# Kernel optimization log

Hardware: AMD Instinct MI355X
Metric: run time of the kernel (lower is better)

## Reference

```python
import jax, jax.numpy as jnp
import numpy as np

N_QUBITS = 12
DIM = 2 ** N_QUBITS  # 4096

_H = (jnp.array([[1.0, 1.0], [1.0, -1.0]]) / np.sqrt(2.0)).astype(jnp.complex64)
_X = jnp.array([[0.0, 1.0], [1.0, 0.0]], dtype=jnp.complex64)


def setup_inputs() -> dict:
    key = jax.random.key(0)
    k1, k2 = jax.random.split(key)
    state = jax.random.normal(k1, (8, 512, DIM), dtype=jnp.float32)
    params = jax.random.normal(k2, (N_QUBITS,), dtype=jnp.float32)
    return {"state": state, "params": params}


def _to_quantum(x):
    # faithful to _classical_to_quantum_inspired: normalize, phase = acos(|v|), sign * exp(i*phase)
    norms = jnp.linalg.norm(x, axis=-1, keepdims=True)
    v = x / (norms + 1e-8)
    mag = jnp.minimum(jnp.abs(v), 1.0)
    q = (jnp.sign(v) * jnp.exp(1j * jnp.arccos(mag))).astype(jnp.complex64)
    nrm = jnp.sqrt(jnp.sum(q.real ** 2 + q.imag ** 2, axis=-1, keepdims=True))
    return q / nrm.astype(jnp.complex64)


def _axis(q):
    # qubit q = bit q (LSB); tensor axes ordered MSB-first after batch axis 0
    return 1 + (N_QUBITS - 1 - q)


def _apply_1q(full, q, U):
    ax = _axis(q)
    moved = jnp.moveaxis(full, ax, -1)
    out = jnp.einsum('...b,ab->...a', moved, U)
    return jnp.moveaxis(out, -1, ax)


def _apply_ctrl(full, c, t, U):
    # apply U on target qubit t where control qubit c == 1
    axc = _axis(c)
    b0 = jnp.take(full, 0, axis=axc)
    b1 = jnp.take(full, 1, axis=axc)
    axt = _axis(t)
    axt_sub = axt - 1 if axt > axc else axt
    moved = jnp.moveaxis(b1, axt_sub, -1)
    b1n = jnp.moveaxis(jnp.einsum('...b,ab->...a', moved, U), -1, axt_sub)
    return jnp.stack([b0, b1n], axis=axc)


def _rx(theta):
    c = jnp.cos(theta / 2).astype(jnp.complex64)
    s = (-1j * jnp.sin(theta / 2)).astype(jnp.complex64)
    return jnp.stack([jnp.stack([c, s]), jnp.stack([s, c])])


def reference(state, params):
    B, T, D = state.shape
    psi = _to_quantum(state.reshape(B * T, D))  # (N, 2**n) complex64
    full = psi.reshape((B * T,) + (2,) * N_QUBITS)
    for q in range(N_QUBITS):
        full = _apply_1q(full, q, _H)                                  # Hadamard
        full = _apply_ctrl(full, q, (q + 1) % N_QUBITS, _rx(params[q]))  # controlled-RX
        if q < N_QUBITS - 1:
            full = _apply_ctrl(full, q, q + 1, _X)                     # CNOT
    amp = full.reshape(B * T, D)
    probs = amp.real ** 2 + amp.imag ** 2  # measurement probabilities
    return probs.reshape(B, T, D).astype(jnp.float32)
```

## Files before the change

kernel.cpp:

```cpp
#include <hip/hip_runtime.h>

#define NQ  12
#define DIM 4096
#define TPB 256

typedef float v2f __attribute__((ext_vector_type(2)));
typedef float v4f __attribute__((ext_vector_type(4)));


__device__ __forceinline__ float wave_reduce(float v) {
#pragma unroll
    for (int m = 32; m >= 1; m >>= 1) v += __shfl_xor(v, m, 64);
    return v;
}

#define BCAST(v, q) __uint_as_float(__builtin_amdgcn_readlane(__float_as_uint(v), (q)))

template <int MC, int MT, bool XGATE>
__device__ __forceinline__ void apply_layer(v2f* a, v2f ctv, v2f snv) {
#pragma unroll
    for (int i = 0; i < 16; ++i) {
        if (i & MC) continue;
        const int j = i | MC;
        const v2f t0 = a[i], t1 = a[j];
        a[i] = t0 + t1;
        a[j] = t0 - t1;
    }
#pragma unroll
    for (int i = 0; i < 16; ++i) {
        if (!(i & MC) || (i & MT)) continue;
        const int j = i | MT;
        const v2f b0 = a[i], b1 = a[j];
        const v2f s0 = snv * b0.yx;
        const v2f s1 = snv * b1.yx;
        if (XGATE) {
            a[i] = ctv * b1 + s0;
            a[j] = ctv * b0 + s1;
        } else {
            a[i] = ctv * b0 + s1;
            a[j] = ctv * b1 + s0;
        }
    }
}

__global__ __launch_bounds__(TPB, 4) void qlayer_kernel(
        const float* __restrict__ state, const float* __restrict__ params,
        float* __restrict__ out) {
    __shared__ __align__(16) v2f amp[DIM + 256];
    __shared__ float red[4];

    const int t = threadIdx.x;
    const int lane = t & 63;
    const long long sbase = (long long)blockIdx.x * DIM;

    const float th = params[lane < NQ ? lane : 0] * 0.5f;
    const float cl = cosf(th);
    const float sl = sinf(th);

    float x[16];
    const float4* gp = (const float4*)(state + sbase + t * 16);
    float ss = 0.f;
#pragma unroll
    for (int j = 0; j < 4; ++j) {
        const float4 v = gp[j];
        x[4 * j + 0] = v.x; x[4 * j + 1] = v.y;
        x[4 * j + 2] = v.z; x[4 * j + 3] = v.w;
        ss = fmaf(v.x, v.x, ss); ss = fmaf(v.y, v.y, ss);
        ss = fmaf(v.z, v.z, ss); ss = fmaf(v.w, v.w, ss);
    }
    ss = wave_reduce(ss);
    if (lane == 0) red[t >> 6] = ss;
    __syncthreads();
    const float nrm  = sqrtf(red[0] + red[1] + red[2] + red[3]);
    const float invd = 1.0f / (nrm + 1e-8f);

    v2f a[16];
#pragma unroll
    for (int k = 0; k < 16; ++k) {
        const float v   = x[k] * invd;
        const float re  = fminf(fmaxf(v, -1.0f), 1.0f);
        const float imb = sqrtf(fmaxf(1.0f - re * re, 0.f));
        const float im  = (v > 0.f) ? imb : ((v < 0.f) ? -imb : 0.f);
        v2f q; q.x = re; q.y = im;
        a[k] = q;
    }

#define CTV(q) ({ v2f _c; _c.x = BCAST(cl, q); _c.y = _c.x; _c; })
#define SNV(q) ({ float _s = BCAST(sl, q); v2f _v; _v.x = _s; _v.y = -_s; _v; })

    apply_layer<1, 2, true>(a, CTV(0), SNV(0));
    apply_layer<2, 4, true>(a, CTV(1), SNV(1));
    apply_layer<4, 8, true>(a, CTV(2), SNV(2));
    {
        const int p1base = 16 * t + 2 * (t >> 1);
#pragma unroll
        for (int k = 0; k < 8; ++k) {
            v4f w; w.x = a[2 * k].x; w.y = a[2 * k].y;
            w.z = a[2 * k + 1].x; w.w = a[2 * k + 1].y;
            *(v4f*)&amp[p1base + 2 * k] = w;
        }
    }
    __syncthreads();

    {
        const int p2base = (t & 7) + 136 * (t >> 3);
#pragma unroll
        for (int r = 0; r < 16; ++r)
            a[r] = amp[p2base + 8 * r + 2 * (r >> 2)];
        apply_layer<1, 2, true>(a, CTV(3), SNV(3));
        apply_layer<2, 4, true>(a, CTV(4), SNV(4));
        apply_layer<4, 8, true>(a, CTV(5), SNV(5));
#pragma unroll
        for (int r = 0; r < 16; ++r)
            amp[p2base + 8 * r + 2 * (r >> 2)] = a[r];
    }
    __syncthreads();

    {
        const int p3base = (t & 63) + 2 * ((t & 63) >> 5) + 1088 * (t >> 6);
#pragma unroll
        for (int r = 0; r < 16; ++r)
            a[r] = amp[p3base + 68 * r];
        apply_layer<1, 2, true>(a, CTV(6), SNV(6));
        apply_layer<2, 4, true>(a, CTV(7), SNV(7));
        apply_layer<4, 8, true>(a, CTV(8), SNV(8));
#pragma unroll
        for (int r = 0; r < 16; ++r)
            amp[p3base + 68 * r] = a[r];
    }
    __syncthreads();

    {
        const int p4base = 2 * t + 2 * (t >> 4);
#pragma unroll
        for (int k = 0; k < 8; ++k) {
            const v4f v = *(const v4f*)&amp[p4base + 544 * k];
            v2f q0; q0.x = v.x; q0.y = v.y;
            v2f q1; q1.x = v.z; q1.y = v.w;
            a[k] = q0;
            a[k + 8] = q1;
        }
        apply_layer<1, 2, true >(a, CTV(9),  SNV(9));
        apply_layer<2, 4, true >(a, CTV(10), SNV(10));
        apply_layer<4, 8, false>(a, CTV(11), SNV(11));

        const float scale = 0x1p-24f;
        float2* outp = (float2*)(out + sbase);
#pragma unroll
        for (int k = 0; k < 8; ++k) {
            const v2f q0 = a[k] * a[k];
            const v2f q1 = a[k | 8] * a[k | 8];
            outp[t + (k << 8)] = make_float2((q0.x + q0.y) * scale,
                                             (q1.x + q1.y) * scale);
        }
    }
#undef CTV
#undef SNV
}

extern "C" void kernel_launch(void* const* d_in, const int* in_sizes, int n_in,
                              void* d_out, int out_size, void* d_ws, size_t ws_size,
                              hipStream_t stream) {
    (void)in_sizes; (void)n_in; (void)out_size; (void)d_ws; (void)ws_size;
    const float* state  = (const float*)d_in[0];
    const float* params = (const float*)d_in[1];
    float* out = (float*)d_out;
    qlayer_kernel<<<dim3(4096), dim3(TPB), 0, stream>>>(state, params, out);
}
```

Before: 121.3 us.

## Redesign shared-memory exchange layout to use 128-bit paired LDS accesses in every stage

Replaces the per-stage shared-memory index maps with a new padded layout (stride 146/1168) so that every exchange between gate stages is done with 16-byte paired stores and loads instead of scalar 8-byte accesses. The in-place read-modify-write per stage becomes read, compute, sync, and write to a permuted location, which adds a barrier per stage. The final output index mapping changes to match the new permutation. The aim is fewer LDS instructions and fewer bank conflicts, at the cost of extra syncs and a larger shared buffer that may reduce occupancy.

```diff
diff --git a/kernel.cpp b/kernel.cpp
--- a/kernel.cpp
+++ b/kernel.cpp
@@ -43,10 +43,21 @@
     }
 }
 
+__device__ __forceinline__ void st_pair(v2f* p, v2f lo, v2f hi) {
+    v4f w; w.x = lo.x; w.y = lo.y; w.z = hi.x; w.w = hi.y;
+    *(v4f*)p = w;
+}
+__device__ __forceinline__ void ld_pair(const v2f* p, v2f* lo, v2f* hi) {
+    const v4f v = *(const v4f*)p;
+    v2f q0; q0.x = v.x; q0.y = v.y;
+    v2f q1; q1.x = v.z; q1.y = v.w;
+    *lo = q0; *hi = q1;
+}
+
 __global__ __launch_bounds__(TPB, 4) void qlayer_kernel(
         const float* __restrict__ state, const float* __restrict__ params,
         float* __restrict__ out) {
-    __shared__ __align__(16) v2f amp[DIM + 256];
+    __shared__ __align__(16) v2f amp[4668];
     __shared__ float red[4];
 
     const int t = threadIdx.x;
@@ -92,66 +103,64 @@
     apply_layer<2, 4, true>(a, CTV(1), SNV(1));
     apply_layer<4, 8, true>(a, CTV(2), SNV(2));
     {
-        const int p1base = 16 * t + 2 * (t >> 1);
+        v2f* wp = &amp[2 * (t & 7) + 146 * (t >> 3)];
 #pragma unroll
-        for (int k = 0; k < 8; ++k) {
-            v4f w; w.x = a[2 * k].x; w.y = a[2 * k].y;
-            w.z = a[2 * k + 1].x; w.w = a[2 * k + 1].y;
-            *(v4f*)&amp[p1base + 2 * k] = w;
-        }
+        for (int k = 0; k < 8; ++k) st_pair(&wp[18 * k], a[k], a[k + 8]);
     }
     __syncthreads();
 
     {
-        const int p2base = (t & 7) + 136 * (t >> 3);
+        const v2f* rp = &amp[18 * (t & 7) + 146 * (t >> 3)];
 #pragma unroll
-        for (int r = 0; r < 16; ++r)
-            a[r] = amp[p2base + 8 * r + 2 * (r >> 2)];
-        apply_layer<1, 2, true>(a, CTV(3), SNV(3));
-        apply_layer<2, 4, true>(a, CTV(4), SNV(4));
-        apply_layer<4, 8, true>(a, CTV(5), SNV(5));
+        for (int m = 0; m < 8; ++m) ld_pair(&rp[2 * m], &a[2 * m], &a[2 * m + 1]);
+    }
+    apply_layer<1, 2, true>(a, CTV(3), SNV(3));
+    apply_layer<2, 4, true>(a, CTV(4), SNV(4));
+    apply_layer<4, 8, true>(a, CTV(5), SNV(5));
+    __syncthreads();
+    {
+        v2f* wp = &amp[2 * ((t >> 3) & 7) + 146 * (t & 7) + 1168 * (t >> 6)];
 #pragma unroll
-        for (int r = 0; r < 16; ++r)
-            amp[p2base + 8 * r + 2 * (r >> 2)] = a[r];
+        for (int k = 0; k < 8; ++k) st_pair(&wp[18 * k], a[k], a[k + 8]);
     }
     __syncthreads();
 
     {
-        const int p3base = (t & 63) + 2 * ((t & 63) >> 5) + 1088 * (t >> 6);
+        const v2f* rp = &amp[18 * (t & 7) + 146 * ((t >> 3) & 7) + 1168 * (t >> 6)];
 #pragma unroll
-        for (int r = 0; r < 16; ++r)
-            a[r] = amp[p3base + 68 * r];
-        apply_layer<1, 2, true>(a, CTV(6), SNV(6));
-        apply_layer<2, 4, true>(a, CTV(7), SNV(7));
-        apply_layer<4, 8, true>(a, CTV(8), SNV(8));
+        for (int m = 0; m < 8; ++m) ld_pair(&rp[2 * m], &a[2 * m], &a[2 * m + 1]);
+    }
+    apply_layer<1, 2, true>(a, CTV(6), SNV(6));
+    apply_layer<2, 4, true>(a, CTV(7), SNV(7));
+    apply_layer<4, 8, true>(a, CTV(8), SNV(8));
+    __syncthreads();
+    {
+        v2f* wp = &amp[2 * (t >> 6) + 8 * ((t >> 3) & 1) + 146 * (t & 7)
+                      + 1168 * ((t >> 4) & 3)];
 #pragma unroll
-        for (int r = 0; r < 16; ++r)
-            amp[p3base + 68 * r] = a[r];
+        for (int k = 0; k < 8; ++k) st_pair(&wp[18 * k], a[k], a[k + 8]);
     }
     __syncthreads();
 
     {
-        const int p4base = 2 * t + 2 * (t >> 4);
+        const v2f* rp = &amp[18 * (t >> 5) + 146 * (t & 7) + 1168 * ((t >> 3) & 3)];
 #pragma unroll
-        for (int k = 0; k < 8; ++k) {
-            const v4f v = *(const v4f*)&amp[p4base + 544 * k];
-            v2f q0; q0.x = v.x; q0.y = v.y;
-            v2f q1; q1.x = v.z; q1.y = v.w;
-            a[k] = q0;
-            a[k + 8] = q1;
-        }
-        apply_layer<1, 2, true >(a, CTV(9),  SNV(9));
-        apply_layer<2, 4, true >(a, CTV(10), SNV(10));
-        apply_layer<4, 8, false>(a, CTV(11), SNV(11));
+        for (int m = 0; m < 8; ++m) ld_pair(&rp[2 * m], &a[2 * m], &a[2 * m + 1]);
+    }
+    apply_layer<1, 2, true >(a, CTV(9),  SNV(9));
+    apply_layer<2, 4, true >(a, CTV(10), SNV(10));
+    apply_layer<4, 8, false>(a, CTV(11), SNV(11));
 
+    {
         const float scale = 0x1p-24f;
         float2* outp = (float2*)(out + sbase);
+        const int obase = ((t >> 3) & 3) + 4 * (t & 7) + 32 * (t >> 5);
 #pragma unroll
         for (int k = 0; k < 8; ++k) {
             const v2f q0 = a[k] * a[k];
             const v2f q1 = a[k | 8] * a[k | 8];
-            outp[t + (k << 8)] = make_float2((q0.x + q0.y) * scale,
-                                             (q1.x + q1.y) * scale);
+            outp[obase + (k << 8)] = make_float2((q0.x + q0.y) * scale,
+                                                 (q1.x + q1.y) * scale);
         }
     }
 #undef CTV
```

Result: no change. 123.3 us (+1.6%).
